# Performance work log

Measured on AMD Instinct MI355X. Metric: run time of the kernel, lower is better.

## Reference

```python
import jax, jax.numpy as jnp
import numpy as np


def setup_inputs() -> dict:
    key = jax.random.key(0)
    kq, kk, kv = jax.random.split(key, 3)
    B, H, S, D = 2, 16, 2048, 64
    return {
        "query": jax.random.normal(kq, (B, H, S, D), dtype=jnp.float32),
        "key": jax.random.normal(kk, (B, H, S, D), dtype=jnp.float32),
        "value": jax.random.normal(kv, (B, H, S, D), dtype=jnp.float32),
    }


def reference(query, key, value):
    # scores = Q K^T / sqrt(d_k)   -> [B, H, S, S]
    d_k = query.shape[-1]
    scale = 1.0 / jnp.sqrt(jnp.asarray(d_k, dtype=query.dtype))
    scores = jnp.einsum("bhqd,bhkd->bhqk", query, key) * scale
    # mask=None path (the module's mask path is unreachable due to a source bug)
    p_attn = jax.nn.softmax(scores, axis=-1)
    out = jnp.einsum("bhqk,bhkd->bhqd", p_attn, value)
    return (out, p_attn)
```

## Files before the change

kernel.cpp:

```cpp
#include <hip/hip_runtime.h>
#include <hip/hip_bf16.h>
#include <cstdint>
#include <cstddef>

#define S_LEN 2048
#define D_HEAD 64
#define NBH 32
#define NELEM 4194304
#define SUP 128

typedef __attribute__((ext_vector_type(8))) short short8;
typedef __attribute__((ext_vector_type(4))) float f32x4;

__device__ __forceinline__ short f2bf(float f) {
    union { float f; uint32_t u; } v; v.f = f;
    uint32_t u = v.u + 0x7FFFu + ((v.u >> 16) & 1u);
    return (short)(u >> 16);
}

__device__ __forceinline__ uint32_t pkbf(float lo, float hi) {
    return ((uint32_t)(uint16_t)f2bf(hi) << 16) | (uint32_t)(uint16_t)f2bf(lo);
}

__global__ void convert_kf_kernel(const float* __restrict__ K, short* __restrict__ Kf) {
    const int s = blockIdx.x * 256 + threadIdx.x;
    const int l = s & 63;
    const int p = (s >> 6) & 1;
    const int g = (s >> 7) & 127;
    const int bh = s >> 14;
    const float* src = K + ((size_t)bh * S_LEN + g * 16 + (l & 15)) * D_HEAD
                         + p * 32 + (l >> 4) * 8;
    short8 y;
    #pragma unroll
    for (int e = 0; e < 8; ++e) y[e] = f2bf(src[e]);
    *reinterpret_cast<short8*>(Kf + (size_t)s * 8) = y;
}

__global__ void transpose_vf_kernel(const float* __restrict__ V, short* __restrict__ Vf) {
    __shared__ float tile[64][65];
    const int bh = blockIdx.y;
    const int s0 = blockIdx.x * 64;
    const int d = threadIdx.x & 63;
    const int r = threadIdx.x >> 6;
    const float* vp = V + ((size_t)bh * S_LEN + s0) * D_HEAD;
    #pragma unroll
    for (int i = 0; i < 16; ++i) {
        int srow = i * 4 + r;
        tile[srow][d] = vp[(size_t)srow * D_HEAD + d];
    }
    __syncthreads();
    #pragma unroll
    for (int h = 0; h < 2; ++h) {
        const int sl = h * 256 + threadIdx.x;
        const int ti = sl >> 8;
        const int vt = (sl >> 6) & 3;
        const int l  = sl & 63;
        const int lrow = l & 15, lgrp = l >> 4;
        short8 y;
        #pragma unroll
        for (int e = 0; e < 8; ++e)
            y[e] = f2bf(tile[ti * 32 + lgrp * 8 + e][vt * 16 + lrow]);
        *reinterpret_cast<short8*>(
            Vf + ((((size_t)bh * 64 + (s0 >> 5) + ti) * 4 + vt) * 64 + l) * 8) = y;
    }
}

__launch_bounds__(256, 2)
__global__ void attn_kernel(const float* __restrict__ Q,
                            const short* __restrict__ Kf,
                            const short* __restrict__ Vf,
                            float* __restrict__ Out,
                            float* __restrict__ P) {
    __shared__ __align__(16) float stage[4][2][16][SUP];

    const int lane = threadIdx.x & 63;
    const int w    = threadIdx.x >> 6;
    const int b    = blockIdx.y * 16 + blockIdx.x;
    const int swzb = (b & 7) * 64 + (b >> 3);
    const int bx   = swzb & 15;
    const int bh   = swzb >> 4;
    const int qb   = bx * 128 + w * 32;
    const int lrow = lane & 15;
    const int lgrp = lane >> 4;
    const float scale = 0.125f;

    short8 qa0A, qa1A, qa0B, qa1B;
    {
        const float* qrA = Q + ((size_t)bh * S_LEN + qb + lrow) * D_HEAD + lgrp * 8;
        const float* qrB = qrA + 16 * D_HEAD;
        #pragma unroll
        for (int e = 0; e < 8; ++e) qa0A[e] = f2bf(qrA[e]);
        #pragma unroll
        for (int e = 0; e < 8; ++e) qa1A[e] = f2bf(qrA[e + 32]);
        #pragma unroll
        for (int e = 0; e < 8; ++e) qa0B[e] = f2bf(qrB[e]);
        #pragma unroll
        for (int e = 0; e < 8; ++e) qa1B[e] = f2bf(qrB[e + 32]);
    }

    const short* Kp = Kf + (size_t)bh * (S_LEN * D_HEAD);
    const short* Vp = Vf + (size_t)bh * (S_LEN * D_HEAD);
    const int lofs = lane * 8;

    const int srcA = ((lane & 15) + ((lane >> 4) & 1) * 32) << 2;
    const int srcB = srcA + (16 << 2);
    const bool glow = (lgrp < 2);

    float lA = 0.f, lB = 0.f;
    f32x4 accA[4] = {}, accB[4] = {};
    for (int j0 = 0; j0 < S_LEN; j0 += 32) {
        const short* kg = Kp + (size_t)(j0 >> 4) * 1024;
        short8 k00 = *reinterpret_cast<const short8*>(kg + lofs);
        short8 k01 = *reinterpret_cast<const short8*>(kg + 512 + lofs);
        short8 k10 = *reinterpret_cast<const short8*>(kg + 1024 + lofs);
        short8 k11 = *reinterpret_cast<const short8*>(kg + 1536 + lofs);
        const short* vg = Vp + (size_t)(j0 >> 5) * 2048;
        short8 bv0 = *reinterpret_cast<const short8*>(vg + lofs);
        short8 bv1 = *reinterpret_cast<const short8*>(vg + 512 + lofs);
        short8 bv2 = *reinterpret_cast<const short8*>(vg + 1024 + lofs);
        short8 bv3 = *reinterpret_cast<const short8*>(vg + 1536 + lofs);

        {
            f32x4 c0 = {0.f, 0.f, 0.f, 0.f};
            f32x4 c1 = {0.f, 0.f, 0.f, 0.f};
            c0 = __builtin_amdgcn_mfma_f32_16x16x32_bf16(k00, qa0A, c0, 0, 0, 0);
            c0 = __builtin_amdgcn_mfma_f32_16x16x32_bf16(k01, qa1A, c0, 0, 0, 0);
            c1 = __builtin_amdgcn_mfma_f32_16x16x32_bf16(k10, qa0A, c1, 0, 0, 0);
            c1 = __builtin_amdgcn_mfma_f32_16x16x32_bf16(k11, qa1A, c1, 0, 0, 0);
            float e0[4], e1[4];
            #pragma unroll
            for (int rr = 0; rr < 4; ++rr) {
                e0[rr] = __expf(c0[rr] * scale);
                e1[rr] = __expf(c1[rr] * scale);
                lA += e0[rr] + e1[rr];
            }
            int w00 = (int)pkbf(e0[0], e0[1]);
            int w01 = (int)pkbf(e0[2], e0[3]);
            int w10 = (int)pkbf(e1[0], e1[1]);
            int w11 = (int)pkbf(e1[2], e1[3]);
            int t0 = __builtin_amdgcn_ds_bpermute(srcA, w00);
            int t1 = __builtin_amdgcn_ds_bpermute(srcA, w01);
            int t2 = __builtin_amdgcn_ds_bpermute(srcB, w00);
            int t3 = __builtin_amdgcn_ds_bpermute(srcB, w01);
            int u0 = __builtin_amdgcn_ds_bpermute(srcA, w10);
            int u1 = __builtin_amdgcn_ds_bpermute(srcA, w11);
            int u2 = __builtin_amdgcn_ds_bpermute(srcB, w10);
            int u3 = __builtin_amdgcn_ds_bpermute(srcB, w11);
            union { short8 s8; int wd[4]; } fr;
            fr.wd[0] = glow ? t0 : u0;
            fr.wd[1] = glow ? t1 : u1;
            fr.wd[2] = glow ? t2 : u2;
            fr.wd[3] = glow ? t3 : u3;
            accA[0] = __builtin_amdgcn_mfma_f32_16x16x32_bf16(fr.s8, bv0, accA[0], 0, 0, 0);
            accA[1] = __builtin_amdgcn_mfma_f32_16x16x32_bf16(fr.s8, bv1, accA[1], 0, 0, 0);
            accA[2] = __builtin_amdgcn_mfma_f32_16x16x32_bf16(fr.s8, bv2, accA[2], 0, 0, 0);
            accA[3] = __builtin_amdgcn_mfma_f32_16x16x32_bf16(fr.s8, bv3, accA[3], 0, 0, 0);
        }
        {
            f32x4 c0 = {0.f, 0.f, 0.f, 0.f};
            f32x4 c1 = {0.f, 0.f, 0.f, 0.f};
            c0 = __builtin_amdgcn_mfma_f32_16x16x32_bf16(k00, qa0B, c0, 0, 0, 0);
            c0 = __builtin_amdgcn_mfma_f32_16x16x32_bf16(k01, qa1B, c0, 0, 0, 0);
            c1 = __builtin_amdgcn_mfma_f32_16x16x32_bf16(k10, qa0B, c1, 0, 0, 0);
            c1 = __builtin_amdgcn_mfma_f32_16x16x32_bf16(k11, qa1B, c1, 0, 0, 0);
            float e0[4], e1[4];
            #pragma unroll
            for (int rr = 0; rr < 4; ++rr) {
                e0[rr] = __expf(c0[rr] * scale);
                e1[rr] = __expf(c1[rr] * scale);
                lB += e0[rr] + e1[rr];
            }
            int w00 = (int)pkbf(e0[0], e0[1]);
            int w01 = (int)pkbf(e0[2], e0[3]);
            int w10 = (int)pkbf(e1[0], e1[1]);
            int w11 = (int)pkbf(e1[2], e1[3]);
            int t0 = __builtin_amdgcn_ds_bpermute(srcA, w00);
            int t1 = __builtin_amdgcn_ds_bpermute(srcA, w01);
            int t2 = __builtin_amdgcn_ds_bpermute(srcB, w00);
            int t3 = __builtin_amdgcn_ds_bpermute(srcB, w01);
            int u0 = __builtin_amdgcn_ds_bpermute(srcA, w10);
            int u1 = __builtin_amdgcn_ds_bpermute(srcA, w11);
            int u2 = __builtin_amdgcn_ds_bpermute(srcB, w10);
            int u3 = __builtin_amdgcn_ds_bpermute(srcB, w11);
            union { short8 s8; int wd[4]; } fr;
            fr.wd[0] = glow ? t0 : u0;
            fr.wd[1] = glow ? t1 : u1;
            fr.wd[2] = glow ? t2 : u2;
            fr.wd[3] = glow ? t3 : u3;
            accB[0] = __builtin_amdgcn_mfma_f32_16x16x32_bf16(fr.s8, bv0, accB[0], 0, 0, 0);
            accB[1] = __builtin_amdgcn_mfma_f32_16x16x32_bf16(fr.s8, bv1, accB[1], 0, 0, 0);
            accB[2] = __builtin_amdgcn_mfma_f32_16x16x32_bf16(fr.s8, bv2, accB[2], 0, 0, 0);
            accB[3] = __builtin_amdgcn_mfma_f32_16x16x32_bf16(fr.s8, bv3, accB[3], 0, 0, 0);
        }
    }
    lA += __shfl_xor(lA, 16);  lA += __shfl_xor(lA, 32);
    lB += __shfl_xor(lB, 16);  lB += __shfl_xor(lB, 32);
    const float rlA = 1.0f / lA;
    const float rlB = 1.0f / lB;

    char* stgA = (char*)&stage[w][0][0][0];
    char* stgB = (char*)&stage[w][1][0][0];
    const int swz = (lrow & 7) << 4;
    float* Pb = P + (size_t)bh * S_LEN * S_LEN;

    for (int sup = 0; sup < S_LEN; sup += SUP) {
        #pragma unroll
        for (int jj = 0; jj < SUP / 32; ++jj) {
            const int j0 = sup + jj * 32;
            const short* kg = Kp + (size_t)(j0 >> 4) * 1024;
            short8 k00 = *reinterpret_cast<const short8*>(kg + lofs);
            short8 k01 = *reinterpret_cast<const short8*>(kg + 512 + lofs);
            short8 k10 = *reinterpret_cast<const short8*>(kg + 1024 + lofs);
            short8 k11 = *reinterpret_cast<const short8*>(kg + 1536 + lofs);
            const int o0 = (lrow * 512 + ((jj * 32 + lgrp * 4) << 2)) ^ swz;
            const int o1 = (lrow * 512 + ((jj * 32 + 16 + lgrp * 4) << 2)) ^ swz;
            {
                f32x4 c0 = {0.f, 0.f, 0.f, 0.f};
                f32x4 c1 = {0.f, 0.f, 0.f, 0.f};
                c0 = __builtin_amdgcn_mfma_f32_16x16x32_bf16(k00, qa0A, c0, 0, 0, 0);
                c0 = __builtin_amdgcn_mfma_f32_16x16x32_bf16(k01, qa1A, c0, 0, 0, 0);
                c1 = __builtin_amdgcn_mfma_f32_16x16x32_bf16(k10, qa0A, c1, 0, 0, 0);
                c1 = __builtin_amdgcn_mfma_f32_16x16x32_bf16(k11, qa1A, c1, 0, 0, 0);
                f32x4 p0, p1;
                #pragma unroll
                for (int rr = 0; rr < 4; ++rr) {
                    p0[rr] = __expf(c0[rr] * scale) * rlA;
                    p1[rr] = __expf(c1[rr] * scale) * rlA;
                }
                *(f32x4*)(stgA + o0) = p0;
                *(f32x4*)(stgA + o1) = p1;
            }
            {
                f32x4 c0 = {0.f, 0.f, 0.f, 0.f};
                f32x4 c1 = {0.f, 0.f, 0.f, 0.f};
                c0 = __builtin_amdgcn_mfma_f32_16x16x32_bf16(k00, qa0B, c0, 0, 0, 0);
                c0 = __builtin_amdgcn_mfma_f32_16x16x32_bf16(k01, qa1B, c0, 0, 0, 0);
                c1 = __builtin_amdgcn_mfma_f32_16x16x32_bf16(k10, qa0B, c1, 0, 0, 0);
                c1 = __builtin_amdgcn_mfma_f32_16x16x32_bf16(k11, qa1B, c1, 0, 0, 0);
                f32x4 p0, p1;
                #pragma unroll
                for (int rr = 0; rr < 4; ++rr) {
                    p0[rr] = __expf(c0[rr] * scale) * rlB;
                    p1[rr] = __expf(c1[rr] * scale) * rlB;
                }
                *(f32x4*)(stgB + o0) = p0;
                *(f32x4*)(stgB + o1) = p1;
            }
        }

        asm volatile("s_waitcnt lgkmcnt(0)" ::: "memory");
        #pragma unroll
        for (int rb = 0; rb < 8; ++rb) {
            const int r = rb * 2 + (lane >> 5);
            const int c = lane & 31;
            f32x4 pv = *(const f32x4*)(stgA + ((r * 512 + c * 16) ^ ((r & 7) << 4)));
            *(f32x4*)(Pb + (size_t)(qb + r) * S_LEN + sup + c * 4) = pv;
        }
        #pragma unroll
        for (int rb = 0; rb < 8; ++rb) {
            const int r = rb * 2 + (lane >> 5);
            const int c = lane & 31;
            f32x4 pv = *(const f32x4*)(stgB + ((r * 512 + c * 16) ^ ((r & 7) << 4)));
            *(f32x4*)(Pb + (size_t)(qb + 16 + r) * S_LEN + sup + c * 4) = pv;
        }
        asm volatile("s_waitcnt lgkmcnt(0)" ::: "memory");
    }

    float rloA[4], rloB[4];
    #pragma unroll
    for (int rr = 0; rr < 4; ++rr) {
        rloA[rr] = __shfl(rlA, lgrp * 4 + rr);
        rloB[rr] = __shfl(rlB, lgrp * 4 + rr);
    }
    float* obA = Out + ((size_t)bh * S_LEN + qb + lgrp * 4) * D_HEAD + lrow;
    float* obB = obA + (size_t)16 * D_HEAD;
    #pragma unroll
    for (int vt = 0; vt < 4; ++vt) {
        #pragma unroll
        for (int rr = 0; rr < 4; ++rr) {
            obA[(size_t)rr * D_HEAD + vt * 16] = accA[vt][rr] * rloA[rr];
            obB[(size_t)rr * D_HEAD + vt * 16] = accB[vt][rr] * rloB[rr];
        }
    }
}

extern "C" void kernel_launch(void* const* d_in, const int* in_sizes, int n_in,
                              void* d_out, int out_size, void* d_ws, size_t ws_size,
                              hipStream_t stream) {
    const float* Q = (const float*)d_in[0];
    const float* K = (const float*)d_in[1];
    const float* V = (const float*)d_in[2];
    float* Out = (float*)d_out;
    float* P = Out + (size_t)NELEM;
    short* Kf = (short*)d_ws;
    short* Vf = Kf + (size_t)NELEM;

    convert_kf_kernel<<<NELEM / (256 * 8), 256, 0, stream>>>(K, Kf);
    transpose_vf_kernel<<<dim3(S_LEN / 64, NBH), 256, 0, stream>>>(V, Vf);
    attn_kernel<<<dim3(S_LEN / 128, NBH), 256, 0, stream>>>(Q, Kf, Vf, Out, P);
}
```

Before: 187.5 us.

## Prefetch next K super-block in registers, use nontemporal P stores, write O early

The second pass (recomputing P and writing it out) now loads the K fragments for the next 128-column super-block into registers while the current block's P rows are being written, which hides global load latency behind the stores. The large P writes use nontemporal stores to avoid polluting cache. The O output is written before the P loop so its accumulator registers can be freed. The prefetch arrays add register pressure, and the last iteration issues one wasted load.

```diff
diff --git a/kernel.cpp b/kernel.cpp
--- a/kernel.cpp
+++ b/kernel.cpp
@@ -198,20 +198,44 @@
     const float rlA = 1.0f / lA;
     const float rlB = 1.0f / lB;
 
+    {
+        float rloA[4], rloB[4];
+        #pragma unroll
+        for (int rr = 0; rr < 4; ++rr) {
+            rloA[rr] = __shfl(rlA, lgrp * 4 + rr);
+            rloB[rr] = __shfl(rlB, lgrp * 4 + rr);
+        }
+        float* obA = Out + ((size_t)bh * S_LEN + qb + lgrp * 4) * D_HEAD + lrow;
+        float* obB = obA + (size_t)16 * D_HEAD;
+        #pragma unroll
+        for (int vt = 0; vt < 4; ++vt) {
+            #pragma unroll
+            for (int rr = 0; rr < 4; ++rr) {
+                obA[(size_t)rr * D_HEAD + vt * 16] = accA[vt][rr] * rloA[rr];
+                obB[(size_t)rr * D_HEAD + vt * 16] = accB[vt][rr] * rloB[rr];
+            }
+        }
+    }
+
     char* stgA = (char*)&stage[w][0][0][0];
     char* stgB = (char*)&stage[w][1][0][0];
     const int swz = (lrow & 7) << 4;
     float* Pb = P + (size_t)bh * S_LEN * S_LEN;
 
+    short8 pk00[4], pk01[4], pk10[4], pk11[4];
+    #pragma unroll
+    for (int jj = 0; jj < 4; ++jj) {
+        const short* kg = Kp + (size_t)((jj * 32) >> 4) * 1024;
+        pk00[jj] = *reinterpret_cast<const short8*>(kg + lofs);
+        pk01[jj] = *reinterpret_cast<const short8*>(kg + 512 + lofs);
+        pk10[jj] = *reinterpret_cast<const short8*>(kg + 1024 + lofs);
+        pk11[jj] = *reinterpret_cast<const short8*>(kg + 1536 + lofs);
+    }
+
     for (int sup = 0; sup < S_LEN; sup += SUP) {
         #pragma unroll
         for (int jj = 0; jj < SUP / 32; ++jj) {
-            const int j0 = sup + jj * 32;
-            const short* kg = Kp + (size_t)(j0 >> 4) * 1024;
-            short8 k00 = *reinterpret_cast<const short8*>(kg + lofs);
-            short8 k01 = *reinterpret_cast<const short8*>(kg + 512 + lofs);
-            short8 k10 = *reinterpret_cast<const short8*>(kg + 1024 + lofs);
-            short8 k11 = *reinterpret_cast<const short8*>(kg + 1536 + lofs);
+            short8 k00 = pk00[jj], k01 = pk01[jj], k10 = pk10[jj], k11 = pk11[jj];
             const int o0 = (lrow * 512 + ((jj * 32 + lgrp * 4) << 2)) ^ swz;
             const int o1 = (lrow * 512 + ((jj * 32 + 16 + lgrp * 4) << 2)) ^ swz;
             {
@@ -249,38 +273,37 @@
         }
 
         asm volatile("s_waitcnt lgkmcnt(0)" ::: "memory");
+
+        {
+            const int nsup = (sup + SUP < S_LEN) ? (sup + SUP) : 0;
+            #pragma unroll
+            for (int jj = 0; jj < 4; ++jj) {
+                const short* kg = Kp + (size_t)((nsup + jj * 32) >> 4) * 1024;
+                pk00[jj] = *reinterpret_cast<const short8*>(kg + lofs);
+                pk01[jj] = *reinterpret_cast<const short8*>(kg + 512 + lofs);
+                pk10[jj] = *reinterpret_cast<const short8*>(kg + 1024 + lofs);
+                pk11[jj] = *reinterpret_cast<const short8*>(kg + 1536 + lofs);
+            }
+        }
+        __builtin_amdgcn_sched_barrier(0);
+
         #pragma unroll
         for (int rb = 0; rb < 8; ++rb) {
             const int r = rb * 2 + (lane >> 5);
             const int c = lane & 31;
             f32x4 pv = *(const f32x4*)(stgA + ((r * 512 + c * 16) ^ ((r & 7) << 4)));
-            *(f32x4*)(Pb + (size_t)(qb + r) * S_LEN + sup + c * 4) = pv;
+            __builtin_nontemporal_store(pv,
+                (f32x4*)(Pb + (size_t)(qb + r) * S_LEN + sup + c * 4));
         }
         #pragma unroll
         for (int rb = 0; rb < 8; ++rb) {
             const int r = rb * 2 + (lane >> 5);
             const int c = lane & 31;
             f32x4 pv = *(const f32x4*)(stgB + ((r * 512 + c * 16) ^ ((r & 7) << 4)));
-            *(f32x4*)(Pb + (size_t)(qb + 16 + r) * S_LEN + sup + c * 4) = pv;
+            __builtin_nontemporal_store(pv,
+                (f32x4*)(Pb + (size_t)(qb + 16 + r) * S_LEN + sup + c * 4));
         }
         asm volatile("s_waitcnt lgkmcnt(0)" ::: "memory");
-    }
-
-    float rloA[4], rloB[4];
-    #pragma unroll
-    for (int rr = 0; rr < 4; ++rr) {
-        rloA[rr] = __shfl(rlA, lgrp * 4 + rr);
-        rloB[rr] = __shfl(rlB, lgrp * 4 + rr);
-    }
-    float* obA = Out + ((size_t)bh * S_LEN + qb + lgrp * 4) * D_HEAD + lrow;
-    float* obB = obA + (size_t)16 * D_HEAD;
-    #pragma unroll
-    for (int vt = 0; vt < 4; ++vt) {
-        #pragma unroll
-        for (int rr = 0; rr < 4; ++rr) {
-            obA[(size_t)rr * D_HEAD + vt * 16] = accA[vt][rr] * rloA[rr];
-            obB[(size_t)rr * D_HEAD + vt * 16] = accB[vt][rr] * rloB[rr];
-        }
     }
 }
 
```

Result: faster. 175.2 us, median of 2 (-6.5%).
